# Optimization experiments

Hardware: AMD Instinct MI355X
Metric: run time of the kernel (lower is better)

The kernel has to match this reference:

```python
import jax, jax.numpy as jnp
import numpy as np

N_NODES = 131072
N_DST = 16384        # batch_size * num_supernodes = 8 * 2048
DEG = 16
N_EDGES = N_DST * DEG
IN_DIM, HID, NDIM = 3, 256, 2
POS_STD = 1.0


def _linear_params(key, fan_in, fan_out):
    # xavier_uniform weights, zero bias; torch Linear stores W as [out, in]
    limit = np.sqrt(6.0 / (fan_in + fan_out)).astype(np.float32)
    w = jax.random.uniform(key, (fan_out, fan_in), jnp.float32, -limit, limit)
    return w, jnp.zeros((fan_out,), jnp.float32)


def setup_inputs() -> dict:
    key = jax.random.key(0)
    ks = jax.random.split(key, 12)
    x = jax.random.normal(ks[0], (N_NODES, IN_DIM), jnp.float32)
    mesh_pos = jax.random.uniform(ks[1], (N_NODES, NDIM), jnp.float32)
    # dst column sorted, each supernode id 0..N_DST-1 appears DEG times (segment_csr layout)
    dst = jnp.repeat(jnp.arange(N_DST, dtype=jnp.int64), DEG)
    src = jax.random.randint(ks[2], (N_EDGES,), 0, N_NODES, jnp.int64)
    mesh_edges = jnp.stack([dst, src], axis=1)  # [E, 2] = (dst, src)
    batch_idx = jnp.repeat(jnp.arange(8, dtype=jnp.int64), N_NODES // 8)
    ip_w1, ip_b1 = _linear_params(ks[3], IN_DIM, HID)
    ip_w2, ip_b2 = _linear_params(ks[4], HID, HID)
    ip_w3, ip_b3 = _linear_params(ks[5], HID, HID)
    msg_w1, msg_b1 = _linear_params(ks[6], 2 * HID, 2 * HID)
    msg_w2, msg_b2 = _linear_params(ks[7], 2 * HID, HID)
    msg_w3, msg_b3 = _linear_params(ks[8], HID, HID)
    b_fourier = jax.random.normal(ks[9], (HID // 2, NDIM), jnp.float32) * POS_STD
    return {
        "x": x, "mesh_pos": mesh_pos, "mesh_edges": mesh_edges, "batch_idx": batch_idx,
        "ip_w1": ip_w1, "ip_b1": ip_b1, "ip_w2": ip_w2, "ip_b2": ip_b2,
        "ip_w3": ip_w3, "ip_b3": ip_b3, "b_fourier": b_fourier,
        "msg_w1": msg_w1, "msg_b1": msg_b1, "msg_w2": msg_w2, "msg_b2": msg_b2,
        "msg_w3": msg_w3, "msg_b3": msg_b3,
        "batch_size": 8, "num_supernodes": 2048,
    }


def reference(x, mesh_pos, mesh_edges, batch_idx,
              ip_w1, ip_b1, ip_w2, ip_b2, ip_w3, ip_b3, b_fourier,
              msg_w1, msg_b1, msg_w2, msg_b2, msg_w3, msg_b3,
              batch_size, num_supernodes):
    gelu = lambda t: jax.nn.gelu(t, approximate=False)  # torch nn.GELU default (erf)
    # input_proj MLP
    h = gelu(x @ ip_w1.T + ip_b1)
    h = gelu(h @ ip_w2.T + ip_b2)
    h = h @ ip_w3.T + ip_b3
    # gaussian sincos positional embedding
    proj = (2.0 * jnp.pi) * (mesh_pos @ b_fourier.T)  # [N, HID/2]
    h = h + jnp.concatenate([jnp.cos(proj), jnp.sin(proj)], axis=-1)
    # edge gather + concat + message MLP
    dst, src = mesh_edges[:, 0], mesh_edges[:, 1]
    m = jnp.concatenate([h[src], h[dst]], axis=1)  # [E, 2*HID]
    m = gelu(m @ msg_w1.T + msg_b1)
    m = gelu(m @ msg_w2.T + msg_b2)
    m = m @ msg_w3.T + msg_b3
    # segment mean over (sorted, compact) destination supernodes
    num_dst = batch_size * num_supernodes
    sums = jax.ops.segment_sum(m, dst, num_segments=num_dst)
    counts = jax.ops.segment_sum(jnp.ones((dst.shape[0],), m.dtype), dst, num_segments=num_dst)
    out = sums / jnp.maximum(counts, 1.0)[:, None]
    return out.reshape(batch_size, num_supernodes, out.shape[-1])
```

## Files before the change

### kernel.cpp

```cpp
#include <hip/hip_runtime.h>
#include <math.h>

#define N_NODES 131072
#define N_DST   16384
#define DEG     16
#define HID     256
#define N_EDGES 262144

typedef __bf16 bf16_8 __attribute__((ext_vector_type(8)));
typedef float  f32_4  __attribute__((ext_vector_type(4)));

__device__ __forceinline__ float gelu_f(float v) {
    float u = fmaf(v * v, -0.10294324f, -2.30220819f) * v;
    float e;
    asm("v_exp_f32 %0, %1" : "=v"(e) : "v"(u));
    return v * __builtin_amdgcn_rcpf(1.0f + e);
}
__device__ __forceinline__ f32_4 zero4() {
    f32_4 z; z[0] = 0.f; z[1] = 0.f; z[2] = 0.f; z[3] = 0.f; return z;
}

__device__ __forceinline__ void load_lds16(const __bf16* g, __bf16* l) {
    __builtin_amdgcn_global_load_lds(
        (__attribute__((address_space(1))) void*)g,
        (__attribute__((address_space(3))) void*)l, 16, 0, 0);
}

__global__ void prep_kernel(__bf16* __restrict__ out,
                            const float* __restrict__ w2,
                            const float* __restrict__ w3,
                            const float* __restrict__ mw1,
                            const float* __restrict__ mw2,
                            const float* __restrict__ mw3) {
    int stride = gridDim.x * blockDim.x;
    for (int i = blockIdx.x * blockDim.x + threadIdx.x; i < 589824; i += stride) {
        float v;
        if      (i <  65536) v = w2[i];
        else if (i < 131072) v = w3[i - 65536];
        else if (i < 393216) v = mw1[i - 131072];
        else if (i < 524288) v = mw2[i - 393216];
        else                 v = mw3[i - 524288];
        out[i] = (__bf16)v;
    }
}

__global__ __launch_bounds__(256) void enc1_kernel(
    const float* __restrict__ x, const float* __restrict__ w1,
    const float* __restrict__ b1, __bf16* __restrict__ h1) {
    const int c8   = threadIdx.x & 31;
    const int nloc = threadIdx.x >> 5;
    float w[24], bb[8];
    #pragma unroll
    for (int i = 0; i < 6; i++) *(float4*)&w[i * 4] = ((const float4*)w1)[c8 * 6 + i];
    *(float4*)&bb[0] = ((const float4*)b1)[c8 * 2 + 0];
    *(float4*)&bb[4] = ((const float4*)b1)[c8 * 2 + 1];
    for (int n = blockIdx.x * 8 + nloc; n < N_NODES; n += gridDim.x * 8) {
        float x0 = x[n * 3 + 0], x1 = x[n * 3 + 1], x2 = x[n * 3 + 2];
        bf16_8 o;
        #pragma unroll
        for (int j = 0; j < 8; j++) {
            float v = fmaf(x2, w[j * 3 + 2],
                      fmaf(x1, w[j * 3 + 1],
                      fmaf(x0, w[j * 3 + 0], bb[j])));
            o[j] = (__bf16)gelu_f(v);
        }
        *(bf16_8*)&h1[(size_t)n * 256 + c8 * 8] = o;
    }
}

__global__ __launch_bounds__(256, 2) void enc23_kernel(
    __bf16* __restrict__ hA,
    const __bf16* __restrict__ W2, const float* __restrict__ b2,
    const __bf16* __restrict__ W3, const float* __restrict__ b3,
    const float* __restrict__ pos, const float* __restrict__ bfour)
{
    __shared__ __align__(16) __bf16 sA[64 * 64];
    __shared__ __align__(16) __bf16 sB[16384];
    __shared__ __align__(16) __bf16 sH2[64 * 256];

    const int tid = threadIdx.x;
    const int m0  = blockIdx.x * 64;
    const int wave = tid >> 6, lane = tid & 63, ln = lane & 15, quad = lane >> 4;
    const int wm = wave >> 1, wn = wave & 1;

    const __bf16* pA[2];
    #pragma unroll
    for (int i = 0; i < 2; i++) {
        int idx = i * 256 + tid;
        int row = idx >> 3, kg = (idx & 7) ^ (row & 7);
        pA[i] = hA + (size_t)(m0 + row) * 256 + kg * 8;
    }

    f32_4 acc[2][8];
    #pragma unroll
    for (int i = 0; i < 2; i++)
        #pragma unroll
        for (int j = 0; j < 8; j++) acc[i][j] = zero4();

    bf16_8 ar[2];
    #pragma unroll
    for (int i = 0; i < 2; i++) ar[i] = *(const bf16_8*)pA[i];

    #pragma unroll
    for (int kb = 0; kb < 4; kb++) {
        if (kb > 0) __syncthreads();
        #pragma unroll
        for (int i = 0; i < 2; i++)
            *(bf16_8*)&sA[(i * 256 + tid) * 8] = ar[i];
        #pragma unroll
        for (int i = 0; i < 8; i++) {
            int idx = i * 256 + tid;
            int row = idx >> 3, kg = (idx & 7) ^ (row & 7);
            load_lds16(W2 + (size_t)row * 256 + kb * 64 + kg * 8, &sB[idx * 8]);
        }
        __syncthreads();
        if (kb < 3) {
            #pragma unroll
            for (int i = 0; i < 2; i++)
                ar[i] = *(const bf16_8*)(pA[i] + (kb + 1) * 64);
        }
        #pragma unroll
        for (int ks = 0; ks < 2; ks++) {
            int c = ks * 4 + quad;
            bf16_8 af[2], bfr[8];
            #pragma unroll
            for (int mt = 0; mt < 2; mt++) {
                int mr = wm * 32 + mt * 16 + ln;
                af[mt] = *(const bf16_8*)&sA[mr * 64 + (c ^ (mr & 7)) * 8];
            }
            #pragma unroll
            for (int nt = 0; nt < 8; nt++) {
                int nr = wn * 128 + nt * 16 + ln;
                bfr[nt] = *(const bf16_8*)&sB[nr * 64 + (c ^ (nr & 7)) * 8];
            }
            #pragma unroll
            for (int mt = 0; mt < 2; mt++)
                #pragma unroll
                for (int nt = 0; nt < 8; nt++)
                    acc[mt][nt] = __builtin_amdgcn_mfma_f32_16x16x32_bf16(af[mt], bfr[nt], acc[mt][nt], 0, 0, 0);
        }
    }
    #pragma unroll
    for (int nt = 0; nt < 8; nt++) {
        int col = wn * 128 + nt * 16 + ln;
        float bb = b2[col];
        #pragma unroll
        for (int mt = 0; mt < 2; mt++) {
            #pragma unroll
            for (int r = 0; r < 4; r++) {
                int row = wm * 32 + mt * 16 + quad * 4 + r;
                sH2[row * 256 + ((col + row * 8) & 255)] = (__bf16)gelu_f(acc[mt][nt][r] + bb);
            }
        }
    }
    #pragma unroll
    for (int i = 0; i < 2; i++)
        #pragma unroll
        for (int j = 0; j < 8; j++) acc[i][j] = zero4();
    __syncthreads();

    #pragma unroll
    for (int kb = 0; kb < 4; kb++) {
        if (kb > 0) __syncthreads();
        #pragma unroll
        for (int i = 0; i < 8; i++) {
            int idx = i * 256 + tid;
            int row = idx >> 3, kg = (idx & 7) ^ (row & 7);
            load_lds16(W3 + (size_t)row * 256 + kb * 64 + kg * 8, &sB[idx * 8]);
        }
        __syncthreads();
        #pragma unroll
        for (int ks = 0; ks < 2; ks++) {
            int c = ks * 4 + quad;
            int k0 = kb * 64 + ks * 32 + quad * 8;
            bf16_8 af[2], bfr[8];
            #pragma unroll
            for (int mt = 0; mt < 2; mt++) {
                int mr = wm * 32 + mt * 16 + ln;
                af[mt] = *(const bf16_8*)&sH2[mr * 256 + ((k0 + mr * 8) & 255)];
            }
            #pragma unroll
            for (int nt = 0; nt < 8; nt++) {
                int nr = wn * 128 + nt * 16 + ln;
                bfr[nt] = *(const bf16_8*)&sB[nr * 64 + (c ^ (nr & 7)) * 8];
            }
            #pragma unroll
            for (int mt = 0; mt < 2; mt++)
                #pragma unroll
                for (int nt = 0; nt < 8; nt++)
                    acc[mt][nt] = __builtin_amdgcn_mfma_f32_16x16x32_bf16(af[mt], bfr[nt], acc[mt][nt], 0, 0, 0);
        }
    }
    __syncthreads();
    __bf16* buf = sB + wave * 4096;
    float b3r[8], Bc0[8], Bc1[8];
    #pragma unroll
    for (int nt = 0; nt < 8; nt++) {
        int col = wn * 128 + nt * 16 + ln;
        b3r[nt] = b3[col];
        int jm = col & 127;
        Bc0[nt] = bfour[jm * 2 + 0];
        Bc1[nt] = bfour[jm * 2 + 1];
    }
    const bool iscos = (wn == 0);
    #pragma unroll
    for (int mt = 0; mt < 2; mt++) {
        #pragma unroll
        for (int r = 0; r < 4; r++) {
            int rowL = mt * 16 + quad * 4 + r;
            int rowE = m0 + wm * 32 + rowL;
            float p0 = pos[rowE * 2 + 0], p1 = pos[rowE * 2 + 1];
            #pragma unroll
            for (int nt = 0; nt < 8; nt++) {
                float f = 6.2831853071795864f * fmaf(p1, Bc1[nt], p0 * Bc0[nt]);
                float v = acc[mt][nt][r] + b3r[nt] + (iscos ? __cosf(f) : __sinf(f));
                int colL = nt * 16 + ln;
                buf[rowL * 128 + ((colL + rowL * 8) & 127)] = (__bf16)v;
            }
        }
    }
    #pragma unroll
    for (int p = 0; p < 8; p++) {
        int rowL = p * 4 + (lane >> 4);
        int c8 = lane & 15;
        bf16_8 vv = *(const bf16_8*)&buf[rowL * 128 + ((c8 * 8 + rowL * 8) & 127)];
        *(bf16_8*)&hA[(size_t)(m0 + wm * 32 + rowL) * 256 + wn * 128 + c8 * 8] = vv;
    }
}

__global__ __launch_bounds__(512, 2) void msg_fused(
    const __bf16* __restrict__ h, const int* __restrict__ edges,
    const __bf16* __restrict__ W1a, const float* __restrict__ b1,
    const __bf16* __restrict__ dmat, const __bf16* __restrict__ W2,
    const float* __restrict__ b2, __bf16* __restrict__ p2)
{
    __shared__ __align__(16) __bf16 sB[2][16384];
    __shared__ __align__(16) __bf16 sM1[16384];

    const int tid = threadIdx.x;
    const int e0  = blockIdx.x * 128;
    const int wave = tid >> 6, lane = tid & 63, ln = lane & 15, quad = lane >> 4;
    const int wm = wave >> 1, wn = wave & 1;

    bf16_8 aA[2][8];
    #pragma unroll
    for (int mt = 0; mt < 2; mt++) {
        int row = wm * 32 + mt * 16 + ln;
        int src = edges[2 * (e0 + row) + 1];
        const __bf16* base = h + (size_t)src * 256 + quad * 8;
        #pragma unroll
        for (int c = 0; c < 8; c++)
            aA[mt][c] = *(const bf16_8*)(base + c * 32);
    }

    int w1e[4], w2e[4];
    #pragma unroll
    for (int i = 0; i < 4; i++) {
        int idx = i * 512 + tid;
        int r1 = idx >> 4, k1 = (idx & 15) ^ (r1 & 7);
        w1e[i] = r1 * 512 + k1 * 8;
        int r2 = idx >> 3, k2 = (idx & 7) ^ (r2 & 7);
        w2e[i] = r2 * 512 + k2 * 8;
    }

    auto stage_w1 = [&](int q, int kb, int p) {
        const __bf16* srcb = W1a + (size_t)q * 128 * 512 + kb * 128;
        #pragma unroll
        for (int i = 0; i < 4; i++)
            load_lds16(srcb + w1e[i], &sB[p][(i * 512 + tid) * 8]);
    };
    auto stage_w2 = [&](int q, int kb2, int p) {
        const __bf16* srcb = W2 + q * 128 + kb2 * 64;
        #pragma unroll
        for (int i = 0; i < 4; i++)
            load_lds16(srcb + w2e[i], &sB[p][(i * 512 + tid) * 8]);
    };

    f32_4 acc2[2][8];
    #pragma unroll
    for (int i = 0; i < 2; i++)
        #pragma unroll
        for (int j = 0; j < 8; j++) acc2[i][j] = zero4();

    stage_w1(0, 0, 0);
    __syncthreads();

    #pragma unroll 1
    for (int q = 0; q < 4; q++) {
        const int colbase = q * 128 + wn * 64;
        float b1r[4], dr[2][4];
        #pragma unroll
        for (int nt = 0; nt < 4; nt++) {
            b1r[nt] = b1[colbase + nt * 16 + ln];
            #pragma unroll
            for (int mt = 0; mt < 2; mt++) {
                int gid = blockIdx.x * 8 + wm * 2 + mt;
                dr[mt][nt] = (float)dmat[(size_t)gid * 512 + colbase + nt * 16 + ln];
            }
        }
        f32_4 acc1[2][4];
        #pragma unroll
        for (int i = 0; i < 2; i++)
            #pragma unroll
            for (int j = 0; j < 4; j++) acc1[i][j] = zero4();

        stage_w1(q, 1, 1);
        #pragma unroll
        for (int ks = 0; ks < 4; ks++) {
            bf16_8 bfr[4];
            #pragma unroll
            for (int nt = 0; nt < 4; nt++) {
                int nr = wn * 64 + nt * 16 + ln;
                bfr[nt] = *(const bf16_8*)&sB[0][nr * 128 + (((ks * 4 + quad) ^ (nr & 7)) * 8)];
            }
            #pragma unroll
            for (int mt = 0; mt < 2; mt++)
                #pragma unroll
                for (int nt = 0; nt < 4; nt++)
                    acc1[mt][nt] = __builtin_amdgcn_mfma_f32_16x16x32_bf16(aA[mt][ks], bfr[nt], acc1[mt][nt], 0, 0, 0);
        }
        __syncthreads();

        stage_w2(q, 0, 0);
        #pragma unroll
        for (int ks = 0; ks < 4; ks++) {
            bf16_8 bfr[4];
            #pragma unroll
            for (int nt = 0; nt < 4; nt++) {
                int nr = wn * 64 + nt * 16 + ln;
                bfr[nt] = *(const bf16_8*)&sB[1][nr * 128 + (((ks * 4 + quad) ^ (nr & 7)) * 8)];
            }
            #pragma unroll
            for (int mt = 0; mt < 2; mt++)
                #pragma unroll
                for (int nt = 0; nt < 4; nt++)
                    acc1[mt][nt] = __builtin_amdgcn_mfma_f32_16x16x32_bf16(aA[mt][4 + ks], bfr[nt], acc1[mt][nt], 0, 0, 0);
        }
        #pragma unroll
        for (int mt = 0; mt < 2; mt++) {
            #pragma unroll
            for (int nt = 0; nt < 4; nt++) {
                #pragma unroll
                for (int r = 0; r < 4; r++) {
                    int row = wm * 32 + mt * 16 + quad * 4 + r;
                    int colq = wn * 64 + nt * 16 + ln;
                    float v = gelu_f(acc1[mt][nt][r] + b1r[nt] + dr[mt][nt]);
                    sM1[row * 128 + ((colq + row * 8) & 127)] = (__bf16)v;
                }
            }
        }
        __syncthreads();

        stage_w2(q, 1, 1);
        #pragma unroll
        for (int ks = 0; ks < 2; ks++) {
            int k0 = ks * 32 + quad * 8;
            bf16_8 af[2], bfr[8];
            #pragma unroll
            for (int mt = 0; mt < 2; mt++) {
                int mr = wm * 32 + mt * 16 + ln;
                af[mt] = *(const bf16_8*)&sM1[mr * 128 + ((k0 + mr * 8) & 127)];
            }
            #pragma unroll
            for (int nt = 0; nt < 8; nt++) {
                int nr = wn * 128 + nt * 16 + ln;
                bfr[nt] = *(const bf16_8*)&sB[0][nr * 64 + (((ks * 4 + quad) ^ (nr & 7)) * 8)];
            }
            #pragma unroll
            for (int mt = 0; mt < 2; mt++)
                #pragma unroll
                for (int nt = 0; nt < 8; nt++)
                    acc2[mt][nt] = __builtin_amdgcn_mfma_f32_16x16x32_bf16(af[mt], bfr[nt], acc2[mt][nt], 0, 0, 0);
        }
        __syncthreads();

        if (q < 3) stage_w1(q + 1, 0, 0);
        #pragma unroll
        for (int ks = 0; ks < 2; ks++) {
            int k0 = 64 + ks * 32 + quad * 8;
            bf16_8 af[2], bfr[8];
            #pragma unroll
            for (int mt = 0; mt < 2; mt++) {
                int mr = wm * 32 + mt * 16 + ln;
                af[mt] = *(const bf16_8*)&sM1[mr * 128 + ((k0 + mr * 8) & 127)];
            }
            #pragma unroll
            for (int nt = 0; nt < 8; nt++) {
                int nr = wn * 128 + nt * 16 + ln;
                bfr[nt] = *(const bf16_8*)&sB[1][nr * 64 + (((ks * 4 + quad) ^ (nr & 7)) * 8)];
            }
            #pragma unroll
            for (int mt = 0; mt < 2; mt++)
                #pragma unroll
                for (int nt = 0; nt < 8; nt++)
                    acc2[mt][nt] = __builtin_amdgcn_mfma_f32_16x16x32_bf16(af[mt], bfr[nt], acc2[mt][nt], 0, 0, 0);
        }
        __syncthreads();
    }

    #pragma unroll
    for (int nt = 0; nt < 8; nt++) {
        int col = wn * 128 + nt * 16 + ln;
        float bb = b2[col];
        #pragma unroll
        for (int mt = 0; mt < 2; mt++) {
            float s = gelu_f(acc2[mt][nt][0] + bb) + gelu_f(acc2[mt][nt][1] + bb)
                    + gelu_f(acc2[mt][nt][2] + bb) + gelu_f(acc2[mt][nt][3] + bb);
            s += __shfl_xor(s, 16);
            s += __shfl_xor(s, 32);
            if (quad == 0) {
                int dstn = edges[2 * (e0 + (wm * 2 + mt) * 16)];
                p2[(size_t)dstn * HID + col] = (__bf16)(s * 0.0625f);
            }
        }
    }
}

template<int K, int GMODE, int WLD, int WOFF, bool BIAS, bool POOL_, bool F32OUT>
__global__ __launch_bounds__(256, 3) void mgemm(
    const __bf16* __restrict__ Ag, const __bf16* __restrict__ h,
    const int* __restrict__ edges, const __bf16* __restrict__ W,
    const float* __restrict__ bias, __bf16* __restrict__ Cb,
    float* __restrict__ Cf, int NB, int Nfull, int e0)
{
    __shared__ __align__(16) __bf16 sA[128 * 64];
    __shared__ __align__(16) __bf16 sB[128 * 64];
    __shared__ int s_idx[128];

    const int tid  = threadIdx.x;
    const int mblk = blockIdx.x / NB;
    const int nblk = blockIdx.x % NB;
    const int m0 = mblk * 128, n0 = nblk * 128;
    const int wave = tid >> 6, lane = tid & 63, ln = lane & 15, quad = lane >> 4;
    const int wm = wave >> 1, wn = wave & 1;

    if (GMODE) {
        if (tid < 128) {
            int r = m0 + tid;
            s_idx[tid] = (GMODE == 1) ? edges[2 * (e0 + r) + 1]
                                      : edges[2 * (DEG * r)];
        }
        __syncthreads();
    }

    const __bf16* pA[4];
    const __bf16* pB[4];
    #pragma unroll
    for (int i = 0; i < 4; i++) {
        int idx = i * 256 + tid;
        int row = idx >> 3, kg = (idx & 7) ^ (row & 7);
        pA[i] = GMODE ? h + (size_t)s_idx[row] * HID + kg * 8
                      : Ag + (size_t)(m0 + row) * K + kg * 8;
        pB[i] = W + (size_t)(n0 + row) * WLD + WOFF + kg * 8;
    }
    const int ach = quad ^ (ln & 7);
    const int aof[2] = { (wm * 64 + ln) * 64 + ach * 8, (wm * 64 + ln) * 64 + (ach ^ 4) * 8 };
    const int bof[2] = { (wn * 64 + ln) * 64 + ach * 8, (wn * 64 + ln) * 64 + (ach ^ 4) * 8 };

    f32_4 acc[4][4];
    #pragma unroll
    for (int i = 0; i < 4; i++)
        #pragma unroll
        for (int j = 0; j < 4; j++) acc[i][j] = zero4();

    bf16_8 ar[4], br[4];
    #pragma unroll
    for (int i = 0; i < 4; i++) {
        ar[i] = *(const bf16_8*)pA[i];
        br[i] = *(const bf16_8*)pB[i];
    }

    #pragma unroll
    for (int kb = 0; kb < K / 64; kb++) {
        if (kb > 0) __syncthreads();
        #pragma unroll
        for (int i = 0; i < 4; i++) {
            int idx = i * 256 + tid;
            *(bf16_8*)&sA[idx * 8] = ar[i];
            *(bf16_8*)&sB[idx * 8] = br[i];
        }
        __syncthreads();
        if (kb + 1 < K / 64) {
            #pragma unroll
            for (int i = 0; i < 4; i++) {
                ar[i] = *(const bf16_8*)(pA[i] + (kb + 1) * 64);
                br[i] = *(const bf16_8*)(pB[i] + (kb + 1) * 64);
            }
        }
        #pragma unroll
        for (int ks = 0; ks < 2; ks++) {
            bf16_8 af[4], bfr[4];
            #pragma unroll
            for (int mt = 0; mt < 4; mt++) af[mt]  = *(const bf16_8*)&sA[aof[ks] + mt * 1024];
            #pragma unroll
            for (int nt = 0; nt < 4; nt++) bfr[nt] = *(const bf16_8*)&sB[bof[ks] + nt * 1024];
            #pragma unroll
            for (int mt = 0; mt < 4; mt++)
                #pragma unroll
                for (int nt = 0; nt < 4; nt++)
                    acc[mt][nt] = __builtin_amdgcn_mfma_f32_16x16x32_bf16(af[mt], bfr[nt], acc[mt][nt], 0, 0, 0);
        }
    }

    if (POOL_) {
        #pragma unroll
        for (int nt = 0; nt < 4; nt++) {
            int col = n0 + wn * 64 + nt * 16 + ln;
            float bb = BIAS ? bias[col] : 0.f;
            #pragma unroll
            for (int mt = 0; mt < 4; mt++) {
                float s = gelu_f(acc[mt][nt][0] + bb) + gelu_f(acc[mt][nt][1] + bb)
                        + gelu_f(acc[mt][nt][2] + bb) + gelu_f(acc[mt][nt][3] + bb);
                s += __shfl_xor(s, 16);
                s += __shfl_xor(s, 32);
                if (quad == 0) {
                    int eg  = e0 + m0 + wm * 64 + mt * 16;
                    int dstn = edges[2 * eg];
                    Cb[(size_t)dstn * HID + col] = (__bf16)(s * 0.0625f);
                }
            }
        }
    } else if (F32OUT) {
        #pragma unroll
        for (int nt = 0; nt < 4; nt++) {
            int col = n0 + wn * 64 + nt * 16 + ln;
            float bb = BIAS ? bias[col] : 0.f;
            #pragma unroll
            for (int mt = 0; mt < 4; mt++) {
                #pragma unroll
                for (int r = 0; r < 4; r++) {
                    int rowE = m0 + wm * 64 + mt * 16 + quad * 4 + r;
                    Cf[(size_t)rowE * Nfull + col] = acc[mt][nt][r] + bb;
                }
            }
        }
    } else {
        __syncthreads();
        __bf16* sw = ((wave & 2) ? sB : sA) + (wave & 1) * 4096;
        #pragma unroll
        for (int nt = 0; nt < 4; nt++) {
            #pragma unroll
            for (int mt = 0; mt < 4; mt++) {
                #pragma unroll
                for (int r = 0; r < 4; r++) {
                    int rowL = mt * 16 + quad * 4 + r;
                    int colL = nt * 16 + ln;
                    sw[rowL * 64 + ((colL + rowL * 8) & 63)] = (__bf16)acc[mt][nt][r];
                }
            }
        }
        __syncthreads();
        #pragma unroll
        for (int p = 0; p < 8; p++) {
            int rowL = p * 8 + (lane >> 3);
            int c8 = lane & 7;
            bf16_8 vv = *(const bf16_8*)&sw[rowL * 64 + ((c8 * 8 + rowL * 8) & 63)];
            int rowE = m0 + wm * 64 + rowL;
            *(bf16_8*)&Cb[(size_t)rowE * Nfull + n0 + wn * 64 + c8 * 8] = vv;
        }
    }
}

extern "C" void kernel_launch(void* const* d_in, const int* in_sizes, int n_in,
                              void* d_out, int out_size, void* d_ws, size_t ws_size,
                              hipStream_t stream) {
    const float* x     = (const float*)d_in[0];
    const float* pos   = (const float*)d_in[1];
    const int*   edges = (const int*)d_in[2];
    const float* ip_w1 = (const float*)d_in[4];
    const float* ip_b1 = (const float*)d_in[5];
    const float* ip_w2 = (const float*)d_in[6];
    const float* ip_b2 = (const float*)d_in[7];
    const float* ip_w3 = (const float*)d_in[8];
    const float* ip_b3 = (const float*)d_in[9];
    const float* bfour = (const float*)d_in[10];
    const float* mw1   = (const float*)d_in[11];
    const float* mb1   = (const float*)d_in[12];
    const float* mw2   = (const float*)d_in[13];
    const float* mb2   = (const float*)d_in[14];
    const float* mw3   = (const float*)d_in[15];
    const float* mb3   = (const float*)d_in[16];

    char* ws = (char*)d_ws;
    __bf16* hA = (__bf16*)ws;
    size_t off = (size_t)N_NODES * HID * 2;
    __bf16* wb = (__bf16*)(ws + off);
    off += (size_t)589824 * 2;
    off = (off + 255) & ~(size_t)255;
    __bf16* dbuf = (__bf16*)(ws + off);
    off += (size_t)N_DST * 512 * 2;
    __bf16* p2 = (__bf16*)(ws + off);
    off += (size_t)N_DST * HID * 2;

    __bf16* w2b  = wb;
    __bf16* w3b  = wb + 65536;
    __bf16* mw1b = wb + 131072;
    __bf16* mw2b = wb + 393216;
    __bf16* mw3b = wb + 524288;

    prep_kernel<<<2304, 256, 0, stream>>>(wb, ip_w2, ip_w3, mw1, mw2, mw3);

    enc1_kernel<<<2048, 256, 0, stream>>>(x, ip_w1, ip_b1, hA);
    enc23_kernel<<<2048, 256, 0, stream>>>(hA, w2b, ip_b2, w3b, ip_b3, pos, bfour);

    mgemm<256, 2, 512, 256, false, false, false><<<512, 256, 0, stream>>>(
        nullptr, hA, edges, mw1b, nullptr, dbuf, nullptr, 4, 512, 0);

    msg_fused<<<2048, 512, 0, stream>>>(hA, edges, mw1b, mb1, dbuf, mw2b, mb2, p2);

    mgemm<256, 0, 256, 0, true, false, true><<<256, 256, 0, stream>>>(
        p2, nullptr, nullptr, mw3b, mb3, nullptr, (float*)d_out, 2, 256, 0);
}
```

Baseline: 448.7 us.

## Triple-buffer weight staging in msg_fused with partial vmcnt waits

Expands the LDS weight staging from two to three buffers and rotates slots so each weight tile is prefetched two phases ahead. Full __syncthreads are replaced by explicit s_waitcnt vmcnt(4) plus s_barrier, so the newest async global-to-LDS loads can stay in flight across barriers. It also pre-adds bias and dmat into one register and switches the launch bounds to an amdgpu_waves_per_eu attribute. The extra 32KB of LDS per block and the hand-written wait counts add occupancy pressure and the risk of ordering mistakes if the compiler emits other memory ops.

```diff
diff --git a/kernel.cpp b/kernel.cpp
--- a/kernel.cpp
+++ b/kernel.cpp
@@ -25,6 +25,11 @@
         (__attribute__((address_space(1))) void*)g,
         (__attribute__((address_space(3))) void*)l, 16, 0, 0);
 }
+
+#define VMW4()  asm volatile("s_waitcnt vmcnt(4)" ::: "memory")
+#define VMW0()  asm volatile("s_waitcnt vmcnt(0)" ::: "memory")
+#define VMW4L() asm volatile("s_waitcnt vmcnt(4) lgkmcnt(0)" ::: "memory")
+#define BAR()   __builtin_amdgcn_s_barrier()
 
 __global__ void prep_kernel(__bf16* __restrict__ out,
                             const float* __restrict__ w2,
@@ -228,13 +233,15 @@
     }
 }
 
-__global__ __launch_bounds__(512, 2) void msg_fused(
+__global__ __launch_bounds__(512)
+__attribute__((amdgpu_waves_per_eu(2, 2)))
+void msg_fused(
     const __bf16* __restrict__ h, const int* __restrict__ edges,
     const __bf16* __restrict__ W1a, const float* __restrict__ b1,
     const __bf16* __restrict__ dmat, const __bf16* __restrict__ W2,
     const float* __restrict__ b2, __bf16* __restrict__ p2)
 {
-    __shared__ __align__(16) __bf16 sB[2][16384];
+    __shared__ __align__(16) __bf16 sB[3][16384];
     __shared__ __align__(16) __bf16 sM1[16384];
 
     const int tid = threadIdx.x;
@@ -253,27 +260,25 @@
             aA[mt][c] = *(const bf16_8*)(base + c * 32);
     }
 
-    int w1e[4], w2e[4];
-    #pragma unroll
-    for (int i = 0; i < 4; i++) {
-        int idx = i * 512 + tid;
-        int r1 = idx >> 4, k1 = (idx & 15) ^ (r1 & 7);
-        w1e[i] = r1 * 512 + k1 * 8;
-        int r2 = idx >> 3, k2 = (idx & 7) ^ (r2 & 7);
-        w2e[i] = r2 * 512 + k2 * 8;
-    }
-
-    auto stage_w1 = [&](int q, int kb, int p) {
-        const __bf16* srcb = W1a + (size_t)q * 128 * 512 + kb * 128;
-        #pragma unroll
-        for (int i = 0; i < 4; i++)
-            load_lds16(srcb + w1e[i], &sB[p][(i * 512 + tid) * 8]);
+    auto stage_w1 = [&](int q, int kb, int slot) {
+        const __bf16* s0 = W1a + (size_t)q * 65536 + kb * 128;
+        __bf16* d = &sB[slot][0];
+        #pragma unroll
+        for (int i = 0; i < 4; i++) {
+            int idx = i * 512 + tid;
+            int r = idx >> 4, kg = (idx & 15) ^ (r & 7);
+            load_lds16(s0 + r * 512 + kg * 8, d + idx * 8);
+        }
     };
-    auto stage_w2 = [&](int q, int kb2, int p) {
-        const __bf16* srcb = W2 + q * 128 + kb2 * 64;
-        #pragma unroll
-        for (int i = 0; i < 4; i++)
-            load_lds16(srcb + w2e[i], &sB[p][(i * 512 + tid) * 8]);
+    auto stage_w2 = [&](int q, int kb2, int slot) {
+        const __bf16* s0 = W2 + q * 128 + kb2 * 64;
+        __bf16* d = &sB[slot][0];
+        #pragma unroll
+        for (int i = 0; i < 4; i++) {
+            int idx = i * 512 + tid;
+            int r = idx >> 3, kg = (idx & 7) ^ (r & 7);
+            load_lds16(s0 + (size_t)r * 512 + kg * 8, d + idx * 8);
+        }
     };
 
     f32_4 acc2[2][8];
@@ -283,19 +288,25 @@
         for (int j = 0; j < 8; j++) acc2[i][j] = zero4();
 
     stage_w1(0, 0, 0);
-    __syncthreads();
-
+    stage_w1(0, 1, 1);
+    VMW4(); BAR();
+
+    int b = 0;
     #pragma unroll 1
     for (int q = 0; q < 4; q++) {
+        const int slA = b;
+        const int slB = (b + 1 >= 3) ? b - 2 : b + 1;
+        const int slC = (b + 2 >= 3) ? b - 1 : b + 2;
+
         const int colbase = q * 128 + wn * 64;
-        float b1r[4], dr[2][4];
+        float bd[2][4];
         #pragma unroll
         for (int nt = 0; nt < 4; nt++) {
-            b1r[nt] = b1[colbase + nt * 16 + ln];
+            float bv = b1[colbase + nt * 16 + ln];
             #pragma unroll
             for (int mt = 0; mt < 2; mt++) {
                 int gid = blockIdx.x * 8 + wm * 2 + mt;
-                dr[mt][nt] = (float)dmat[(size_t)gid * 512 + colbase + nt * 16 + ln];
+                bd[mt][nt] = bv + (float)dmat[(size_t)gid * 512 + colbase + nt * 16 + ln];
             }
         }
         f32_4 acc1[2][4];
@@ -304,14 +315,14 @@
             #pragma unroll
             for (int j = 0; j < 4; j++) acc1[i][j] = zero4();
 
-        stage_w1(q, 1, 1);
+        stage_w2(q, 0, slC);
         #pragma unroll
         for (int ks = 0; ks < 4; ks++) {
             bf16_8 bfr[4];
             #pragma unroll
             for (int nt = 0; nt < 4; nt++) {
                 int nr = wn * 64 + nt * 16 + ln;
-                bfr[nt] = *(const bf16_8*)&sB[0][nr * 128 + (((ks * 4 + quad) ^ (nr & 7)) * 8)];
+                bfr[nt] = *(const bf16_8*)&sB[slA][nr * 128 + (((ks * 4 + quad) ^ (nr & 7)) * 8)];
             }
             #pragma unroll
             for (int mt = 0; mt < 2; mt++)
@@ -319,16 +330,16 @@
                 for (int nt = 0; nt < 4; nt++)
                     acc1[mt][nt] = __builtin_amdgcn_mfma_f32_16x16x32_bf16(aA[mt][ks], bfr[nt], acc1[mt][nt], 0, 0, 0);
         }
-        __syncthreads();
-
-        stage_w2(q, 0, 0);
+        VMW4(); BAR();
+
+        stage_w2(q, 1, slA);
         #pragma unroll
         for (int ks = 0; ks < 4; ks++) {
             bf16_8 bfr[4];
             #pragma unroll
             for (int nt = 0; nt < 4; nt++) {
                 int nr = wn * 64 + nt * 16 + ln;
-                bfr[nt] = *(const bf16_8*)&sB[1][nr * 128 + (((ks * 4 + quad) ^ (nr & 7)) * 8)];
+                bfr[nt] = *(const bf16_8*)&sB[slB][nr * 128 + (((ks * 4 + quad) ^ (nr & 7)) * 8)];
             }
             #pragma unroll
             for (int mt = 0; mt < 2; mt++)
@@ -344,14 +355,14 @@
                 for (int r = 0; r < 4; r++) {
                     int row = wm * 32 + mt * 16 + quad * 4 + r;
                     int colq = wn * 64 + nt * 16 + ln;
-                    float v = gelu_f(acc1[mt][nt][r] + b1r[nt] + dr[mt][nt]);
+                    float v = gelu_f(acc1[mt][nt][r] + bd[mt][nt]);
                     sM1[row * 128 + ((colq + row * 8) & 127)] = (__bf16)v;
                 }
             }
         }
-        __syncthreads();
-
-        stage_w2(q, 1, 1);
+        VMW4L(); BAR();
+
+        if (q < 3) stage_w1(q + 1, 0, slB);
         #pragma unroll
         for (int ks = 0; ks < 2; ks++) {
             int k0 = ks * 32 + quad * 8;
@@ -364,7 +375,7 @@
             #pragma unroll
             for (int nt = 0; nt < 8; nt++) {
                 int nr = wn * 128 + nt * 16 + ln;
-                bfr[nt] = *(const bf16_8*)&sB[0][nr * 64 + (((ks * 4 + quad) ^ (nr & 7)) * 8)];
+                bfr[nt] = *(const bf16_8*)&sB[slC][nr * 64 + (((ks * 4 + quad) ^ (nr & 7)) * 8)];
             }
             #pragma unroll
             for (int mt = 0; mt < 2; mt++)
@@ -372,9 +383,10 @@
                 for (int nt = 0; nt < 8; nt++)
                     acc2[mt][nt] = __builtin_amdgcn_mfma_f32_16x16x32_bf16(af[mt], bfr[nt], acc2[mt][nt], 0, 0, 0);
         }
-        __syncthreads();
-
-        if (q < 3) stage_w1(q + 1, 0, 0);
+        if (q < 3) { VMW4(); } else { VMW0(); }
+        BAR();
+
+        if (q < 3) stage_w1(q + 1, 1, slC);
         #pragma unroll
         for (int ks = 0; ks < 2; ks++) {
             int k0 = 64 + ks * 32 + quad * 8;
@@ -387,7 +399,7 @@
             #pragma unroll
             for (int nt = 0; nt < 8; nt++) {
                 int nr = wn * 128 + nt * 16 + ln;
-                bfr[nt] = *(const bf16_8*)&sB[1][nr * 64 + (((ks * 4 + quad) ^ (nr & 7)) * 8)];
+                bfr[nt] = *(const bf16_8*)&sB[slA][nr * 64 + (((ks * 4 + quad) ^ (nr & 7)) * 8)];
             }
             #pragma unroll
             for (int mt = 0; mt < 2; mt++)
@@ -395,7 +407,8 @@
                 for (int nt = 0; nt < 8; nt++)
                     acc2[mt][nt] = __builtin_amdgcn_mfma_f32_16x16x32_bf16(af[mt], bfr[nt], acc2[mt][nt], 0, 0, 0);
         }
-        __syncthreads();
+        if (q < 3) { VMW4(); BAR(); }
+        b = slB;
     }
 
     #pragma unroll
```

After: 499.6 us. 11.3% more time.

## Stage gathered source rows in LDS via async loads; fold msg bias into dst GEMM

Applied to the files above, without the earlier changes.

The msg_fused kernel now gathers the 128 source-node rows into a swizzled LDS buffer with global_load_lds instead of holding them in registers, and reads A fragments from LDS. Launch bounds drop to one block per CU because LDS use rises to 160KB. The first message bias is folded into the precomputed dst-term GEMM epilogue, before its bf16 rounding, so msg_fused no longer loads b1. This is meant to cut register pressure and make the gather asynchronous, at the cost of lower occupancy and extra LDS traffic.

```diff
diff --git a/kernel.cpp b/kernel.cpp
--- a/kernel.cpp
+++ b/kernel.cpp
@@ -228,12 +228,13 @@
     }
 }
 
-__global__ __launch_bounds__(512, 2) void msg_fused(
+__global__ __launch_bounds__(512, 1) void msg_fused(
     const __bf16* __restrict__ h, const int* __restrict__ edges,
-    const __bf16* __restrict__ W1a, const float* __restrict__ b1,
-    const __bf16* __restrict__ dmat, const __bf16* __restrict__ W2,
-    const float* __restrict__ b2, __bf16* __restrict__ p2)
+    const __bf16* __restrict__ W1a, const __bf16* __restrict__ dmat,
+    const __bf16* __restrict__ W2, const float* __restrict__ b2,
+    __bf16* __restrict__ p2)
 {
+    __shared__ __align__(16) __bf16 sH[32768];
     __shared__ __align__(16) __bf16 sB[2][16384];
     __shared__ __align__(16) __bf16 sM1[16384];
 
@@ -242,60 +243,54 @@
     const int wave = tid >> 6, lane = tid & 63, ln = lane & 15, quad = lane >> 4;
     const int wm = wave >> 1, wn = wave & 1;
 
-    bf16_8 aA[2][8];
-    #pragma unroll
-    for (int mt = 0; mt < 2; mt++) {
-        int row = wm * 32 + mt * 16 + ln;
-        int src = edges[2 * (e0 + row) + 1];
-        const __bf16* base = h + (size_t)src * 256 + quad * 8;
-        #pragma unroll
-        for (int c = 0; c < 8; c++)
-            aA[mt][c] = *(const bf16_8*)(base + c * 32);
-    }
-
-    int w1e[4], w2e[4];
-    #pragma unroll
-    for (int i = 0; i < 4; i++) {
-        int idx = i * 512 + tid;
-        int r1 = idx >> 4, k1 = (idx & 15) ^ (r1 & 7);
-        w1e[i] = r1 * 512 + k1 * 8;
-        int r2 = idx >> 3, k2 = (idx & 7) ^ (r2 & 7);
-        w2e[i] = r2 * 512 + k2 * 8;
-    }
+    int* s_src = (int*)sM1;
+    if (tid < 128) s_src[tid] = edges[2 * (e0 + tid) + 1];
+    __syncthreads();
 
     auto stage_w1 = [&](int q, int kb, int p) {
-        const __bf16* srcb = W1a + (size_t)q * 128 * 512 + kb * 128;
-        #pragma unroll
-        for (int i = 0; i < 4; i++)
-            load_lds16(srcb + w1e[i], &sB[p][(i * 512 + tid) * 8]);
+        const __bf16* s0 = W1a + (size_t)(q * 128) * 512 + kb * 128;
+        #pragma unroll
+        for (int i = 0; i < 4; i++) {
+            int idx = i * 512 + tid;
+            int r = idx >> 4, kg = (idx & 15) ^ (r & 7);
+            load_lds16(s0 + r * 512 + kg * 8, &sB[p][idx * 8]);
+        }
     };
     auto stage_w2 = [&](int q, int kb2, int p) {
-        const __bf16* srcb = W2 + q * 128 + kb2 * 64;
-        #pragma unroll
-        for (int i = 0; i < 4; i++)
-            load_lds16(srcb + w2e[i], &sB[p][(i * 512 + tid) * 8]);
+        const __bf16* s0 = W2 + q * 128 + kb2 * 64;
+        #pragma unroll
+        for (int i = 0; i < 4; i++) {
+            int idx = i * 512 + tid;
+            int r = idx >> 3, kg = (idx & 7) ^ (r & 7);
+            load_lds16(s0 + (size_t)r * 512 + kg * 8, &sB[p][idx * 8]);
+        }
     };
 
-    f32_4 acc2[2][8];
-    #pragma unroll
-    for (int i = 0; i < 2; i++)
-        #pragma unroll
-        for (int j = 0; j < 8; j++) acc2[i][j] = zero4();
-
+    #pragma unroll
+    for (int i = 0; i < 8; i++) {
+        int idx = i * 512 + tid;
+        int row = idx >> 5, kg = (idx & 31) ^ (row & 7);
+        load_lds16(h + (size_t)s_src[row] * 256 + kg * 8, &sH[idx * 8]);
+    }
     stage_w1(0, 0, 0);
     __syncthreads();
+
+    f32_4 acc2[2][8];
+    #pragma unroll
+    for (int i = 0; i < 2; i++)
+        #pragma unroll
+        for (int j = 0; j < 8; j++) acc2[i][j] = zero4();
 
     #pragma unroll 1
     for (int q = 0; q < 4; q++) {
         const int colbase = q * 128 + wn * 64;
-        float b1r[4], dr[2][4];
+        float bd[2][4];
         #pragma unroll
         for (int nt = 0; nt < 4; nt++) {
-            b1r[nt] = b1[colbase + nt * 16 + ln];
             #pragma unroll
             for (int mt = 0; mt < 2; mt++) {
                 int gid = blockIdx.x * 8 + wm * 2 + mt;
-                dr[mt][nt] = (float)dmat[(size_t)gid * 512 + colbase + nt * 16 + ln];
+                bd[mt][nt] = (float)dmat[(size_t)gid * 512 + colbase + nt * 16 + ln];
             }
         }
         f32_4 acc1[2][4];
@@ -307,34 +302,47 @@
         stage_w1(q, 1, 1);
         #pragma unroll
         for (int ks = 0; ks < 4; ks++) {
-            bf16_8 bfr[4];
+            int c = ks * 4 + quad;
+            bf16_8 af[2], bfr[4];
+            #pragma unroll
+            for (int mt = 0; mt < 2; mt++) {
+                int mr = wm * 32 + mt * 16 + ln;
+                af[mt] = *(const bf16_8*)&sH[mr * 256 + ((c ^ (mr & 7)) * 8)];
+            }
             #pragma unroll
             for (int nt = 0; nt < 4; nt++) {
                 int nr = wn * 64 + nt * 16 + ln;
-                bfr[nt] = *(const bf16_8*)&sB[0][nr * 128 + (((ks * 4 + quad) ^ (nr & 7)) * 8)];
+                bfr[nt] = *(const bf16_8*)&sB[0][nr * 128 + ((c ^ (nr & 7)) * 8)];
             }
             #pragma unroll
             for (int mt = 0; mt < 2; mt++)
                 #pragma unroll
                 for (int nt = 0; nt < 4; nt++)
-                    acc1[mt][nt] = __builtin_amdgcn_mfma_f32_16x16x32_bf16(aA[mt][ks], bfr[nt], acc1[mt][nt], 0, 0, 0);
+                    acc1[mt][nt] = __builtin_amdgcn_mfma_f32_16x16x32_bf16(af[mt], bfr[nt], acc1[mt][nt], 0, 0, 0);
         }
         __syncthreads();
 
         stage_w2(q, 0, 0);
         #pragma unroll
         for (int ks = 0; ks < 4; ks++) {
-            bf16_8 bfr[4];
+            int cb = ks * 4 + quad;
+            int ca = 16 + cb;
+            bf16_8 af[2], bfr[4];
+            #pragma unroll
+            for (int mt = 0; mt < 2; mt++) {
+                int mr = wm * 32 + mt * 16 + ln;
+                af[mt] = *(const bf16_8*)&sH[mr * 256 + ((ca ^ (mr & 7)) * 8)];
+            }
             #pragma unroll
             for (int nt = 0; nt < 4; nt++) {
                 int nr = wn * 64 + nt * 16 + ln;
-                bfr[nt] = *(const bf16_8*)&sB[1][nr * 128 + (((ks * 4 + quad) ^ (nr & 7)) * 8)];
+                bfr[nt] = *(const bf16_8*)&sB[1][nr * 128 + ((cb ^ (nr & 7)) * 8)];
             }
             #pragma unroll
             for (int mt = 0; mt < 2; mt++)
                 #pragma unroll
                 for (int nt = 0; nt < 4; nt++)
-                    acc1[mt][nt] = __builtin_amdgcn_mfma_f32_16x16x32_bf16(aA[mt][4 + ks], bfr[nt], acc1[mt][nt], 0, 0, 0);
+                    acc1[mt][nt] = __builtin_amdgcn_mfma_f32_16x16x32_bf16(af[mt], bfr[nt], acc1[mt][nt], 0, 0, 0);
         }
         #pragma unroll
         for (int mt = 0; mt < 2; mt++) {
@@ -344,7 +352,7 @@
                 for (int r = 0; r < 4; r++) {
                     int row = wm * 32 + mt * 16 + quad * 4 + r;
                     int colq = wn * 64 + nt * 16 + ln;
-                    float v = gelu_f(acc1[mt][nt][r] + b1r[nt] + dr[mt][nt]);
+                    float v = gelu_f(acc1[mt][nt][r] + bd[mt][nt]);
                     sM1[row * 128 + ((colq + row * 8) & 127)] = (__bf16)v;
                 }
             }
@@ -355,6 +363,7 @@
         #pragma unroll
         for (int ks = 0; ks < 2; ks++) {
             int k0 = ks * 32 + quad * 8;
+            int cb2 = ks * 4 + quad;
             bf16_8 af[2], bfr[8];
             #pragma unroll
             for (int mt = 0; mt < 2; mt++) {
@@ -364,7 +373,7 @@
             #pragma unroll
             for (int nt = 0; nt < 8; nt++) {
                 int nr = wn * 128 + nt * 16 + ln;
-                bfr[nt] = *(const bf16_8*)&sB[0][nr * 64 + (((ks * 4 + quad) ^ (nr & 7)) * 8)];
+                bfr[nt] = *(const bf16_8*)&sB[0][nr * 64 + ((cb2 ^ (nr & 7)) * 8)];
             }
             #pragma unroll
             for (int mt = 0; mt < 2; mt++)
@@ -378,6 +387,7 @@
         #pragma unroll
         for (int ks = 0; ks < 2; ks++) {
             int k0 = 64 + ks * 32 + quad * 8;
+            int cb2 = ks * 4 + quad;
             bf16_8 af[2], bfr[8];
             #pragma unroll
             for (int mt = 0; mt < 2; mt++) {
@@ -387,7 +397,7 @@
             #pragma unroll
             for (int nt = 0; nt < 8; nt++) {
                 int nr = wn * 128 + nt * 16 + ln;
-                bfr[nt] = *(const bf16_8*)&sB[1][nr * 64 + (((ks * 4 + quad) ^ (nr & 7)) * 8)];
+                bfr[nt] = *(const bf16_8*)&sB[1][nr * 64 + ((cb2 ^ (nr & 7)) * 8)];
             }
             #pragma unroll
             for (int mt = 0; mt < 2; mt++)
@@ -539,13 +549,14 @@
         __bf16* sw = ((wave & 2) ? sB : sA) + (wave & 1) * 4096;
         #pragma unroll
         for (int nt = 0; nt < 4; nt++) {
+            float bb = BIAS ? bias[n0 + wn * 64 + nt * 16 + ln] : 0.f;
             #pragma unroll
             for (int mt = 0; mt < 4; mt++) {
                 #pragma unroll
                 for (int r = 0; r < 4; r++) {
                     int rowL = mt * 16 + quad * 4 + r;
                     int colL = nt * 16 + ln;
-                    sw[rowL * 64 + ((colL + rowL * 8) & 63)] = (__bf16)acc[mt][nt][r];
+                    sw[rowL * 64 + ((colL + rowL * 8) & 63)] = (__bf16)(acc[mt][nt][r] + bb);
                 }
             }
         }
@@ -603,10 +614,10 @@
     enc1_kernel<<<2048, 256, 0, stream>>>(x, ip_w1, ip_b1, hA);
     enc23_kernel<<<2048, 256, 0, stream>>>(hA, w2b, ip_b2, w3b, ip_b3, pos, bfour);
 
-    mgemm<256, 2, 512, 256, false, false, false><<<512, 256, 0, stream>>>(
-        nullptr, hA, edges, mw1b, nullptr, dbuf, nullptr, 4, 512, 0);
-
-    msg_fused<<<2048, 512, 0, stream>>>(hA, edges, mw1b, mb1, dbuf, mw2b, mb2, p2);
+    mgemm<256, 2, 512, 256, true, false, false><<<512, 256, 0, stream>>>(
+        nullptr, hA, edges, mw1b, mb1, dbuf, nullptr, 4, 512, 0);
+
+    msg_fused<<<2048, 512, 0, stream>>>(hA, edges, mw1b, dbuf, mw2b, mb2, p2);
 
     mgemm<256, 0, 256, 0, true, false, true><<<256, 256, 0, stream>>>(
         p2, nullptr, nullptr, mw3b, mb3, nullptr, (float*)d_out, 2, 256, 0);
```

After: 419.9 us. -6.4%, faster.
